# Kernel tuning notes

Hardware: AMD Instinct MI355X
Metric: run time of the kernel (lower is better)

The kernel has to match this reference:

```python
import jax, jax.numpy as jnp
import numpy as np

N = 10000
E = 160000
D = 512
EPS = 1e-5


def _lin_params(key, out_d, in_d, bias=True):
    k1, k2 = jax.random.split(key)
    s = 1.0 / np.sqrt(in_d)
    W = jax.random.uniform(k1, (out_d, in_d), jnp.float32, -s, s)
    if bias:
        b = jax.random.uniform(k2, (out_d,), jnp.float32, -s, s)
        return W, b
    return (W,)


def setup_inputs() -> dict:
    key = jax.random.key(0)
    ks = jax.random.split(key, 16)
    inp = {
        "x": jax.random.normal(ks[0], (N, D), jnp.float32),
        "edge_index": jax.random.randint(ks[1], (2, E), 0, N, jnp.int64),
    }
    ki = 2
    for l in range(3):
        Wp, bp = _lin_params(ks[ki], D, D); ki += 1
        Wl, bl = _lin_params(ks[ki], D, D); ki += 1
        (Wr,) = _lin_params(ks[ki], D, D, bias=False); ki += 1
        inp[f"Wp{l}"] = Wp; inp[f"bp{l}"] = bp
        inp[f"Wl{l}"] = Wl; inp[f"bl{l}"] = bl
        inp[f"Wr{l}"] = Wr
        if l < 2:  # ReLU+LayerNorm between convs
            inp[f"g{l}"] = jnp.ones((D,), jnp.float32)
            inp[f"be{l}"] = jnp.zeros((D,), jnp.float32)
    return inp


def _sage_conv(x, src, dst, Wp, bp, Wl, bl, Wr):
    # PyG SAGEConv with project=True: project+ReLU messages, mean-aggregate, lin_l + lin_r(root)
    h = jax.nn.relu(x @ Wp.T + bp)                      # [N, D] projected messages
    agg = jax.ops.segment_sum(h[src], dst, num_segments=N)   # gather + scatter-add
    cnt = jax.ops.segment_sum(jnp.ones((src.shape[0],), x.dtype), dst, num_segments=N)
    agg = agg / jnp.maximum(cnt, 1.0)[:, None]          # mean over incoming edges
    return agg @ Wl.T + bl + x @ Wr.T


def _relu_ln(x, g, b):
    x = jax.nn.relu(x)
    mu = jnp.mean(x, axis=-1, keepdims=True)
    var = jnp.mean(jnp.square(x - mu), axis=-1, keepdims=True)
    return (x - mu) * jax.lax.rsqrt(var + EPS) * g + b


def reference(x, edge_index,
              Wp0, bp0, Wl0, bl0, Wr0, g0, be0,
              Wp1, bp1, Wl1, bl1, Wr1, g1, be1,
              Wp2, bp2, Wl2, bl2, Wr2):
    src, dst = edge_index[0], edge_index[1]
    x = _sage_conv(x, src, dst, Wp0, bp0, Wl0, bl0, Wr0)
    x = _relu_ln(x, g0, be0)
    x = _sage_conv(x, src, dst, Wp1, bp1, Wl1, bl1, Wr1)
    x = _relu_ln(x, g1, be1)
    x = _sage_conv(x, src, dst, Wp2, bp2, Wl2, bl2, Wr2)
    return x
```

## Files before the change

kernel.cpp:

```cpp
#include <hip/hip_runtime.h>
#include <cstdint>

#define D 512
#define TM 128
#define TN 128
#define BK 32
#define CAP 64

typedef unsigned short u16;
typedef __bf16 bf16x8 __attribute__((ext_vector_type(8)));
typedef float f32x4 __attribute__((ext_vector_type(4)));

__device__ __forceinline__ float bf2f(u16 u) {
    unsigned int x = ((unsigned int)u) << 16;
    return __builtin_bit_cast(float, x);
}
__device__ __forceinline__ u16 f2bf(float f) {
    unsigned int x = __builtin_bit_cast(unsigned int, f);
    x += 0x7fffu + ((x >> 16) & 1u);
    return (u16)(x >> 16);
}

__device__ __forceinline__ void gload16(const u16* g, u16* l) {
    __builtin_amdgcn_global_load_lds(
        (const __attribute__((address_space(1))) void*)(uintptr_t)g,
        (__attribute__((address_space(3))) void*)(unsigned int)(uintptr_t)l,
        16, 0, 0);
}

__device__ __forceinline__ bool is_bf16(const u16* xraw) {
    int lane = threadIdx.x & 63;
    u16 u = xraw[2 * lane];
    int e = (u >> 7) & 0xFF;
    unsigned long long b = __ballot(e >= 110 && e <= 129);
    return __popcll(b) >= 32;
}
__device__ __forceinline__ bool is_i64(const int* eraw) {
    int lane = threadIdx.x & 63;
    unsigned long long b = __ballot(eraw[2 * lane + 1] == 0);
    return __popcll(b) >= 32;
}

__global__ __launch_bounds__(256) void convert_x(
    const void* __restrict__ src, u16* __restrict__ out)
{
    bool bf = is_bf16((const u16*)src);
    int i = (blockIdx.x * 256 + threadIdx.x) * 8;
    if (bf) {
        *(uint4*)(out + i) = *(const uint4*)((const u16*)src + i);
    } else {
        const float* f = (const float*)src + i;
        float4 a = *(const float4*)f;
        float4 b = *(const float4*)(f + 4);
        u16 r[8] = {f2bf(a.x), f2bf(a.y), f2bf(a.z), f2bf(a.w),
                    f2bf(b.x), f2bf(b.y), f2bf(b.z), f2bf(b.w)};
        *(uint4*)(out + i) = *(uint4*)r;
    }
}

struct Ptrs9  { const void* p[9];  };
struct Ptrs10 { const void* p[10]; };

__global__ __launch_bounds__(256) void convert_wb(
    Ptrs9 s, Ptrs10 v, u16* __restrict__ wout, float* __restrict__ vout,
    const u16* __restrict__ xraw)
{
    bool bf = is_bf16(xraw);
    int m = blockIdx.y;
    if (m < 9) {
        const void* src = s.p[m];
        u16* o = wout + (size_t)m * D * D;
        int i = (blockIdx.x * 256 + threadIdx.x) * 8;
        if (bf) {
            *(uint4*)(o + i) = *(const uint4*)((const u16*)src + i);
        } else {
            const float* f = (const float*)src + i;
            float4 a = *(const float4*)f;
            float4 b = *(const float4*)(f + 4);
            u16 r[8] = {f2bf(a.x), f2bf(a.y), f2bf(a.z), f2bf(a.w),
                        f2bf(b.x), f2bf(b.y), f2bf(b.z), f2bf(b.w)};
            *(uint4*)(o + i) = *(uint4*)r;
        }
    } else if (blockIdx.x == 0) {
        for (int b = 0; b < 10; b++) {
            const void* src = v.p[b];
            for (int j = threadIdx.x * 2; j < threadIdx.x * 2 + 2; j++) {
                float val = bf ? bf2f(((const u16*)src)[j]) : ((const float*)src)[j];
                vout[b * 512 + j] = val;
            }
        }
    }
}

__global__ void build_bucket(const int* __restrict__ eraw,
                             int* __restrict__ cnt, u16* __restrict__ bucket,
                             int E, int Nn)
{
    bool i64 = is_i64(eraw);
    int e = blockIdx.x * 256 + threadIdx.x;
    if (e < E) {
        int s, d;
        if (i64) { s = eraw[2 * e]; d = eraw[2 * (E + e)]; }
        else     { s = eraw[e];     d = eraw[E + e]; }
        s = min(max(s, 0), Nn - 1);
        d = min(max(d, 0), Nn - 1);
        int p = atomicAdd(&cnt[d], 1);
        if (p < CAP) bucket[(size_t)d * CAP + p] = (u16)s;
    }
}

template <int NPASS, bool RELU, bool FINAL>
__global__ __launch_bounds__(256) void gemm_bt(
    const u16* __restrict__ A0, const u16* __restrict__ B0,
    const u16* __restrict__ A1, const u16* __restrict__ B1,
    const float* __restrict__ bias, void* __restrict__ Cout,
    const u16* __restrict__ xraw, int M)
{
    __shared__ __align__(16) u16 sA[TM * BK];
    __shared__ __align__(16) u16 sB[TN * BK];

    const int t    = threadIdx.x;
    const int m0   = blockIdx.x * TM;
    const int n0   = blockIdx.y * TN;
    const int wave = t >> 6, lane = t & 63;
    const int wm   = wave >> 1, wn = wave & 1;
    const int lrow = lane & 15, quad = lane >> 4;

    const bool out_bf16 = FINAL ? is_bf16(xraw) : true;

    f32x4 acc[4][4];
#pragma unroll
    for (int i = 0; i < 4; i++)
#pragma unroll
        for (int j = 0; j < 4; j++)
#pragma unroll
            for (int r = 0; r < 4; r++) acc[i][j][r] = 0.f;

    const int cA  = (t & 3) * 8;
    const int rA0 = min(m0 + (t >> 2),      M - 1);
    const int rA1 = min(m0 + 64 + (t >> 2), M - 1);
    const int rB0 = n0 + (t >> 2);
    const int rB1 = n0 + 64 + (t >> 2);

#pragma unroll 1
    for (int p = 0; p < NPASS; p++) {
        const u16* A = p ? A1 : A0;
        const u16* B = p ? B1 : B0;
        const u16* gA0 = A + (size_t)rA0 * D + cA;
        const u16* gA1 = A + (size_t)rA1 * D + cA;
        const u16* gB0 = B + (size_t)rB0 * D + cA;
        const u16* gB1 = B + (size_t)rB1 * D + cA;

#pragma unroll 1
        for (int k0 = 0; k0 < D; k0 += BK) {
            gload16(gA0 + k0, &sA[(size_t)t * 8]);
            gload16(gA1 + k0, &sA[(size_t)(t + 256) * 8]);
            gload16(gB0 + k0, &sB[(size_t)t * 8]);
            gload16(gB1 + k0, &sB[(size_t)(t + 256) * 8]);
            __syncthreads();

            bf16x8 af[4], bfr[4];
#pragma unroll
            for (int mi = 0; mi < 4; mi++)
                af[mi] = *(const bf16x8*)&sA[(wm * 64 + mi * 16 + lrow) * BK + quad * 8];
#pragma unroll
            for (int ni = 0; ni < 4; ni++)
                bfr[ni] = *(const bf16x8*)&sB[(wn * 64 + ni * 16 + lrow) * BK + quad * 8];
#pragma unroll
            for (int mi = 0; mi < 4; mi++)
#pragma unroll
                for (int ni = 0; ni < 4; ni++)
                    acc[mi][ni] = __builtin_amdgcn_mfma_f32_16x16x32_bf16(
                        af[mi], bfr[ni], acc[mi][ni], 0, 0, 0);
            __syncthreads();
        }
    }

#pragma unroll
    for (int ni = 0; ni < 4; ni++) {
        int col = n0 + wn * 64 + ni * 16 + lrow;
        float bv = bias[col];
#pragma unroll
        for (int mi = 0; mi < 4; mi++) {
            int row0 = m0 + wm * 64 + mi * 16 + quad * 4;
#pragma unroll
            for (int r = 0; r < 4; r++) {
                int row = row0 + r;
                if (row < M) {
                    float v = acc[mi][ni][r] + bv;
                    if (RELU) v = fmaxf(v, 0.f);
                    if (!FINAL || out_bf16)
                        ((u16*)Cout)[(size_t)row * D + col] = f2bf(v);
                    else
                        ((float*)Cout)[(size_t)row * D + col] = v;
                }
            }
        }
    }
}

__global__ __launch_bounds__(256) void aggregate(
    const u16* __restrict__ h, const int* __restrict__ cnt,
    const u16* __restrict__ bucket, u16* __restrict__ agg, int M)
{
    const int w = threadIdx.x >> 6, lane = threadIdx.x & 63;
    const int n = blockIdx.x * 4 + w;

    __shared__ u16 sidx[4][CAP];
    int deg = 0, dd = 0;
    if (n < M) {
        deg = cnt[n];
        dd  = min(deg, CAP);
        if (lane < dd) sidx[w][lane] = bucket[(size_t)n * CAP + lane];
    }
    __syncthreads();
    if (n >= M) return;

    float a[8] = {0.f, 0.f, 0.f, 0.f, 0.f, 0.f, 0.f, 0.f};
    int i = 0;
    for (; i + 4 <= dd; i += 4) {
        uint4 v0 = *(const uint4*)(h + (size_t)sidx[w][i]     * D + lane * 8);
        uint4 v1 = *(const uint4*)(h + (size_t)sidx[w][i + 1] * D + lane * 8);
        uint4 v2 = *(const uint4*)(h + (size_t)sidx[w][i + 2] * D + lane * 8);
        uint4 v3 = *(const uint4*)(h + (size_t)sidx[w][i + 3] * D + lane * 8);
        const unsigned int* u0 = (const unsigned int*)&v0;
        const unsigned int* u1 = (const unsigned int*)&v1;
        const unsigned int* u2 = (const unsigned int*)&v2;
        const unsigned int* u3 = (const unsigned int*)&v3;
#pragma unroll
        for (int j = 0; j < 4; j++) {
            a[2 * j]     += bf2f((u16)(u0[j] & 0xffffu)) + bf2f((u16)(u1[j] & 0xffffu))
                          + bf2f((u16)(u2[j] & 0xffffu)) + bf2f((u16)(u3[j] & 0xffffu));
            a[2 * j + 1] += bf2f((u16)(u0[j] >> 16)) + bf2f((u16)(u1[j] >> 16))
                          + bf2f((u16)(u2[j] >> 16)) + bf2f((u16)(u3[j] >> 16));
        }
    }
    for (; i < dd; i++) {
        uint4 v0 = *(const uint4*)(h + (size_t)sidx[w][i] * D + lane * 8);
        const unsigned int* u0 = (const unsigned int*)&v0;
#pragma unroll
        for (int j = 0; j < 4; j++) {
            a[2 * j]     += bf2f((u16)(u0[j] & 0xffffu));
            a[2 * j + 1] += bf2f((u16)(u0[j] >> 16));
        }
    }

    float inv = 1.f / fmaxf((float)deg, 1.f);
    u16 r[8];
#pragma unroll
    for (int j = 0; j < 8; j++) r[j] = f2bf(a[j] * inv);
    *(uint4*)(agg + (size_t)n * D + lane * 8) = *(uint4*)r;
}

__global__ __launch_bounds__(256) void relu_ln(
    const u16* __restrict__ y, const float* __restrict__ g, const float* __restrict__ be,
    u16* __restrict__ out, int M)
{
    const int row  = blockIdx.x * 4 + (threadIdx.x >> 6);
    const int lane = threadIdx.x & 63;
    if (row >= M) return;

    typedef short s16x8 __attribute__((ext_vector_type(8)));
    s16x8 v = *(const s16x8*)(y + (size_t)row * D + lane * 8);
    float f[8], s = 0.f, s2 = 0.f;
#pragma unroll
    for (int i = 0; i < 8; i++) {
        float x = bf2f((u16)v[i]);
        x = fmaxf(x, 0.f);
        f[i] = x; s += x; s2 += x * x;
    }
#pragma unroll
    for (int off = 32; off >= 1; off >>= 1) {
        s  += __shfl_xor(s, off);
        s2 += __shfl_xor(s2, off);
    }
    float mean = s * (1.f / 512.f);
    float var  = s2 * (1.f / 512.f) - mean * mean;
    float rstd = rsqrtf(var + 1e-5f);

    s16x8 res;
#pragma unroll
    for (int i = 0; i < 8; i++) {
        float o = (f[i] - mean) * rstd * g[lane * 8 + i] + be[lane * 8 + i];
        res[i] = (short)f2bf(o);
    }
    *(s16x8*)(out + (size_t)row * D + lane * 8) = res;
}

extern "C" void kernel_launch(void* const* d_in, const int* in_sizes, int n_in,
                              void* d_out, int out_size, void* d_ws, size_t ws_size,
                              hipStream_t stream)
{
    const int M = in_sizes[0] / D;
    const int E = in_sizes[1] / 2;
    const void* xraw = d_in[0];
    const int*  eraw = (const int*)d_in[1];

    const void *Wp[3], *bp[3], *Wl[3], *bl[3], *Wr[3], *g[2], *be[2];
    int idx = 2;
    for (int l = 0; l < 3; l++) {
        Wp[l] = d_in[idx++]; bp[l] = d_in[idx++];
        Wl[l] = d_in[idx++]; bl[l] = d_in[idx++];
        Wr[l] = d_in[idx++];
        if (l < 2) { g[l] = d_in[idx++]; be[l] = d_in[idx++]; }
    }

    char* w = (char*)d_ws;
    auto alloc = [&](size_t bytes) { void* p = w; w += (bytes + 255) & ~(size_t)255; return p; };
    u16*   xb     = (u16*)  alloc((size_t)M * D * 2);
    u16*   h      = (u16*)  alloc((size_t)M * D * 2);
    u16*   agg    = (u16*)  alloc((size_t)M * D * 2);
    u16*   Wb     = (u16*)  alloc((size_t)9 * D * D * 2);
    float* vecf   = (float*)alloc((size_t)10 * 512 * 4);
    int*   cnt    = (int*)  alloc((size_t)M * 4);
    u16*   bucket = (u16*)  alloc((size_t)M * CAP * 2);

    convert_x<<<dim3(M * D / (256 * 8)), dim3(256), 0, stream>>>(xraw, xb);

    Ptrs9 mats;
    const void* morder[9] = {Wp[0], Wl[0], Wr[0], Wp[1], Wl[1], Wr[1], Wp[2], Wl[2], Wr[2]};
    for (int i = 0; i < 9; i++) mats.p[i] = morder[i];
    Ptrs10 vecs;
    const void* vorder[10] = {bp[0], bl[0], g[0], be[0], bp[1], bl[1], g[1], be[1], bp[2], bl[2]};
    for (int i = 0; i < 10; i++) vecs.p[i] = vorder[i];
    convert_wb<<<dim3(D * D / (256 * 8), 10), dim3(256), 0, stream>>>(
        mats, vecs, Wb, vecf, (const u16*)xraw);

    hipMemsetAsync(cnt, 0, (size_t)M * 4, stream);
    build_bucket<<<dim3((E + 255) / 256), dim3(256), 0, stream>>>(eraw, cnt, bucket, E, M);

    const u16* WM[9]; for (int i = 0; i < 9; i++) WM[i] = Wb + (size_t)i * D * D;
    const float* VB[10]; for (int i = 0; i < 10; i++) VB[i] = vecf + (size_t)i * 512;

    u16* yb = (u16*)d_out;
    dim3 gg((M + TM - 1) / TM, D / TN);
    const u16* xin = xb;
    for (int l = 0; l < 3; l++) {
        gemm_bt<1, true, false><<<gg, dim3(256), 0, stream>>>(
            xin, WM[l * 3 + 0], xin, WM[l * 3 + 0], VB[l * 4 + 0], h, (const u16*)xraw, M);
        aggregate<<<dim3((M + 3) / 4), dim3(256), 0, stream>>>(h, cnt, bucket, agg, M);
        if (l < 2) {
            gemm_bt<2, false, false><<<gg, dim3(256), 0, stream>>>(
                agg, WM[l * 3 + 1], xin, WM[l * 3 + 2], VB[l * 4 + 1], yb, (const u16*)xraw, M);
            relu_ln<<<dim3((M + 3) / 4), dim3(256), 0, stream>>>(
                yb, VB[l * 4 + 2], VB[l * 4 + 3], xb, M);
            xin = xb;
        } else {
            gemm_bt<2, false, true><<<gg, dim3(256), 0, stream>>>(
                agg, WM[l * 3 + 1], xin, WM[l * 3 + 2], VB[l * 4 + 1], d_out, (const u16*)xraw, M);
        }
    }
}
```

Measured before the change: 381.0 us.

## Fold LayerNorm into next-layer weights and fuse prep kernels

Removes the separate relu_ln kernel. The gamma scale is folded into the next layer's Wp and Wr weights, and beta is folded into bias vectors computed in a prep pass. The ReLU'd output of the second GEMM is stored together with per-row sum and sum-of-squares gathered through atomics, and the next GEMMs apply mean and rstd in their epilogue. It also merges the x conversion, weight conversion and edge bucketing into one grid-stride prep kernel, and halves TN to 64 for more blocks. The costs are row-stat atomics, a serial 512-length dot per thread in prep, and a change in numerics, since LN is now applied after a bf16 GEMM on un-normalized inputs.

```diff
diff --git a/kernel.cpp b/kernel.cpp
--- a/kernel.cpp
+++ b/kernel.cpp
@@ -3,7 +3,7 @@
 
 #define D 512
 #define TM 128
-#define TN 128
+#define TN 64
 #define BK 32
 #define CAP 64
 
@@ -20,14 +20,15 @@
     x += 0x7fffu + ((x >> 16) & 1u);
     return (u16)(x >> 16);
 }
-
+__device__ __forceinline__ float loadf(const void* p, int i, bool bf) {
+    return bf ? bf2f(((const u16*)p)[i]) : ((const float*)p)[i];
+}
 __device__ __forceinline__ void gload16(const u16* g, u16* l) {
     __builtin_amdgcn_global_load_lds(
         (const __attribute__((address_space(1))) void*)(uintptr_t)g,
         (__attribute__((address_space(3))) void*)(unsigned int)(uintptr_t)l,
         16, 0, 0);
 }
-
 __device__ __forceinline__ bool is_bf16(const u16* xraw) {
     int lane = threadIdx.x & 63;
     u16 u = xraw[2 * lane];
@@ -41,80 +42,108 @@
     return __popcll(b) >= 32;
 }
 
-__global__ __launch_bounds__(256) void convert_x(
-    const void* __restrict__ src, u16* __restrict__ out)
+struct PrepArgs {
+    const u16* xraw; const int* eraw;
+    const void* W[9];
+    const void* V[10];
+    u16* xb; u16* Wb; float* vecf;
+    int* cnt; u16* bucket;
+    int M, E;
+};
+
+__global__ __launch_bounds__(256) void prep(PrepArgs a)
 {
-    bool bf = is_bf16((const u16*)src);
-    int i = (blockIdx.x * 256 + threadIdx.x) * 8;
-    if (bf) {
-        *(uint4*)(out + i) = *(const uint4*)((const u16*)src + i);
-    } else {
-        const float* f = (const float*)src + i;
-        float4 a = *(const float4*)f;
-        float4 b = *(const float4*)(f + 4);
-        u16 r[8] = {f2bf(a.x), f2bf(a.y), f2bf(a.z), f2bf(a.w),
-                    f2bf(b.x), f2bf(b.y), f2bf(b.z), f2bf(b.w)};
-        *(uint4*)(out + i) = *(uint4*)r;
-    }
-}
-
-struct Ptrs9  { const void* p[9];  };
-struct Ptrs10 { const void* p[10]; };
-
-__global__ __launch_bounds__(256) void convert_wb(
-    Ptrs9 s, Ptrs10 v, u16* __restrict__ wout, float* __restrict__ vout,
-    const u16* __restrict__ xraw)
-{
-    bool bf = is_bf16(xraw);
-    int m = blockIdx.y;
-    if (m < 9) {
-        const void* src = s.p[m];
-        u16* o = wout + (size_t)m * D * D;
-        int i = (blockIdx.x * 256 + threadIdx.x) * 8;
+    const bool bf  = is_bf16(a.xraw);
+    const bool i64 = is_i64(a.eraw);
+    const int gt = blockIdx.x * 256 + threadIdx.x;
+    const int gs = gridDim.x * 256;
+
+    const int nx = a.M * D / 8;
+    for (int i = gt; i < nx; i += gs) {
         if (bf) {
-            *(uint4*)(o + i) = *(const uint4*)((const u16*)src + i);
+            *(uint4*)(a.xb + i * 8) = *(const uint4*)(a.xraw + i * 8);
         } else {
-            const float* f = (const float*)src + i;
-            float4 a = *(const float4*)f;
-            float4 b = *(const float4*)(f + 4);
-            u16 r[8] = {f2bf(a.x), f2bf(a.y), f2bf(a.z), f2bf(a.w),
-                        f2bf(b.x), f2bf(b.y), f2bf(b.z), f2bf(b.w)};
-            *(uint4*)(o + i) = *(uint4*)r;
-        }
-    } else if (blockIdx.x == 0) {
-        for (int b = 0; b < 10; b++) {
-            const void* src = v.p[b];
-            for (int j = threadIdx.x * 2; j < threadIdx.x * 2 + 2; j++) {
-                float val = bf ? bf2f(((const u16*)src)[j]) : ((const float*)src)[j];
-                vout[b * 512 + j] = val;
-            }
-        }
-    }
-}
-
-__global__ void build_bucket(const int* __restrict__ eraw,
-                             int* __restrict__ cnt, u16* __restrict__ bucket,
-                             int E, int Nn)
-{
-    bool i64 = is_i64(eraw);
-    int e = blockIdx.x * 256 + threadIdx.x;
-    if (e < E) {
+            const float* f = (const float*)a.xraw + i * 8;
+            float4 p = *(const float4*)f, q = *(const float4*)(f + 4);
+            u16 r[8] = {f2bf(p.x), f2bf(p.y), f2bf(p.z), f2bf(p.w),
+                        f2bf(q.x), f2bf(q.y), f2bf(q.z), f2bf(q.w)};
+            *(uint4*)(a.xb + i * 8) = *(uint4*)r;
+        }
+    }
+
+    for (int i = gt; i < 9 * 32768; i += gs) {
+        int m = i >> 15, j = i & 32767;
+        const void* gsrc = nullptr;
+        if (m == 3 || m == 5) gsrc = a.V[2];
+        else if (m == 6 || m == 8) gsrc = a.V[6];
+        const void* src = a.W[m];
+        int c0 = (j * 8) & 511;
+        float v[8];
+        if (bf) {
+            const u16* s = (const u16*)src + j * 8;
+#pragma unroll
+            for (int e = 0; e < 8; e++) v[e] = bf2f(s[e]);
+        } else {
+            const float* s = (const float*)src + j * 8;
+#pragma unroll
+            for (int e = 0; e < 8; e++) v[e] = s[e];
+        }
+        if (gsrc) {
+#pragma unroll
+            for (int e = 0; e < 8; e++) v[e] *= loadf(gsrc, c0 + e, bf);
+        }
+        u16 r[8];
+#pragma unroll
+        for (int e = 0; e < 8; e++) r[e] = f2bf(v[e]);
+        *(uint4*)(a.Wb + (size_t)m * D * D + j * 8) = *(uint4*)r;
+    }
+
+    for (int e = gt; e < 10 * 512; e += gs) {
+        int t = e >> 9, n = e & 511;
+        float outv;
+        if (t == 0)      outv = loadf(a.V[0], n, bf);
+        else if (t == 1) outv = loadf(a.V[1], n, bf);
+        else {
+            int q = t - 2;
+            const int wi[8] = {3, 3, 5, 5, 6, 6, 8, 8};
+            const void* wraw = a.W[wi[q]];
+            const void* dotv = (q < 4) ? ((q & 1) ? a.V[3] : a.V[2])
+                                       : ((q & 1) ? a.V[7] : a.V[6]);
+            float acc = 0.f;
+            if (bf) {
+                const u16* wr = (const u16*)wraw + (size_t)n * 512;
+                for (int k = 0; k < 512; k++) acc += bf2f(wr[k]) * loadf(dotv, k, bf);
+            } else {
+                const float* wr = (const float*)wraw + (size_t)n * 512;
+                for (int k = 0; k < 512; k++) acc += wr[k] * loadf(dotv, k, bf);
+            }
+            if (q & 1) {
+                const void* braw = (q == 1) ? a.V[4] : (q == 3) ? a.V[5]
+                                 : (q == 5) ? a.V[8] : a.V[9];
+                acc += loadf(braw, n, bf);
+            }
+            outv = acc;
+        }
+        a.vecf[t * 512 + n] = outv;
+    }
+
+    for (int e2 = gt; e2 < a.E; e2 += gs) {
         int s, d;
-        if (i64) { s = eraw[2 * e]; d = eraw[2 * (E + e)]; }
-        else     { s = eraw[e];     d = eraw[E + e]; }
-        s = min(max(s, 0), Nn - 1);
-        d = min(max(d, 0), Nn - 1);
-        int p = atomicAdd(&cnt[d], 1);
-        if (p < CAP) bucket[(size_t)d * CAP + p] = (u16)s;
-    }
-}
-
-template <int NPASS, bool RELU, bool FINAL>
-__global__ __launch_bounds__(256) void gemm_bt(
-    const u16* __restrict__ A0, const u16* __restrict__ B0,
-    const u16* __restrict__ A1, const u16* __restrict__ B1,
-    const float* __restrict__ bias, void* __restrict__ Cout,
-    const u16* __restrict__ xraw, int M)
+        if (i64) { s = a.eraw[2 * e2]; d = a.eraw[2 * (a.E + e2)]; }
+        else     { s = a.eraw[e2];     d = a.eraw[a.E + e2]; }
+        s = min(max(s, 0), a.M - 1);
+        d = min(max(d, 0), a.M - 1);
+        int p = atomicAdd(&a.cnt[d], 1);
+        if (p < CAP) a.bucket[(size_t)d * CAP + p] = (u16)s;
+    }
+}
+
+template <bool LNIN>
+__global__ __launch_bounds__(256) void gemm1k(
+    const u16* __restrict__ A, const u16* __restrict__ W,
+    const float* __restrict__ bias, const float* __restrict__ svec,
+    const float* __restrict__ mu, const float* __restrict__ m2,
+    u16* __restrict__ hout, int M)
 {
     __shared__ __align__(16) u16 sA[TM * BK];
     __shared__ __align__(16) u16 sB[TN * BK];
@@ -126,73 +155,212 @@
     const int wm   = wave >> 1, wn = wave & 1;
     const int lrow = lane & 15, quad = lane >> 4;
 
+    float rstd[4][4], nmu[4][4];
+    if (LNIN) {
+#pragma unroll
+        for (int mi = 0; mi < 4; mi++)
+#pragma unroll
+            for (int r = 0; r < 4; r++) {
+                int row = min(m0 + wm * 64 + mi * 16 + quad * 4 + r, M - 1);
+                float mean = mu[row] * (1.f / 512.f);
+                float var  = m2[row] * (1.f / 512.f) - mean * mean;
+                float rs   = rsqrtf(fmaxf(var, 0.f) + 1e-5f);
+                rstd[mi][r] = rs;
+                nmu[mi][r]  = -mean * rs;
+            }
+    }
+
+    f32x4 acc[4][2];
+#pragma unroll
+    for (int i = 0; i < 4; i++)
+#pragma unroll
+        for (int j = 0; j < 2; j++)
+#pragma unroll
+            for (int r = 0; r < 4; r++) acc[i][j][r] = 0.f;
+
+    const int cA    = (t & 3) * 8;
+    const int rowA0 = min(m0 + (t >> 2),      M - 1);
+    const int rowA1 = min(m0 + 64 + (t >> 2), M - 1);
+    const int rowB  = n0 + (t >> 2);
+    const u16* gA0 = A + (size_t)rowA0 * D + cA;
+    const u16* gA1 = A + (size_t)rowA1 * D + cA;
+    const u16* gB  = W + (size_t)rowB  * D + cA;
+
+#pragma unroll 1
+    for (int k0 = 0; k0 < D; k0 += BK) {
+        gload16(gA0 + k0, &sA[(size_t)t * 8]);
+        gload16(gA1 + k0, &sA[(size_t)(t + 256) * 8]);
+        gload16(gB  + k0, &sB[(size_t)t * 8]);
+        __syncthreads();
+        bf16x8 af[4], bfr[2];
+#pragma unroll
+        for (int mi = 0; mi < 4; mi++)
+            af[mi] = *(const bf16x8*)&sA[(wm * 64 + mi * 16 + lrow) * BK + quad * 8];
+#pragma unroll
+        for (int ni = 0; ni < 2; ni++)
+            bfr[ni] = *(const bf16x8*)&sB[(wn * 32 + ni * 16 + lrow) * BK + quad * 8];
+#pragma unroll
+        for (int mi = 0; mi < 4; mi++)
+#pragma unroll
+            for (int ni = 0; ni < 2; ni++)
+                acc[mi][ni] = __builtin_amdgcn_mfma_f32_16x16x32_bf16(
+                    af[mi], bfr[ni], acc[mi][ni], 0, 0, 0);
+        __syncthreads();
+    }
+
+#pragma unroll
+    for (int ni = 0; ni < 2; ni++) {
+        int col = n0 + wn * 32 + ni * 16 + lrow;
+        float bv = bias[col];
+        float sv = LNIN ? svec[col] : 0.f;
+#pragma unroll
+        for (int mi = 0; mi < 4; mi++) {
+            int row0 = m0 + wm * 64 + mi * 16 + quad * 4;
+#pragma unroll
+            for (int r = 0; r < 4; r++) {
+                int row = row0 + r;
+                if (row < M) {
+                    float v = LNIN ? rstd[mi][r] * acc[mi][ni][r] + nmu[mi][r] * sv + bv
+                                   : acc[mi][ni][r] + bv;
+                    hout[(size_t)row * D + col] = f2bf(fmaxf(v, 0.f));
+                }
+            }
+        }
+    }
+}
+
+template <bool LNIN, bool STATS, bool FINAL>
+__global__ __launch_bounds__(256) void gemm2k(
+    const u16* __restrict__ A0, const u16* __restrict__ W0,
+    const u16* __restrict__ A1, const u16* __restrict__ W1,
+    const float* __restrict__ bias, const float* __restrict__ s2vec,
+    const float* __restrict__ mu_in, const float* __restrict__ m2_in,
+    float* __restrict__ mu_out, float* __restrict__ m2_out,
+    void* __restrict__ out, const u16* __restrict__ xraw, int M)
+{
+    __shared__ __align__(16) u16 sA[TM * BK];
+    __shared__ __align__(16) u16 sB[TN * BK];
+
+    const int t    = threadIdx.x;
+    const int m0   = blockIdx.x * TM;
+    const int n0   = blockIdx.y * TN;
+    const int wave = t >> 6, lane = t & 63;
+    const int wm   = wave >> 1, wn = wave & 1;
+    const int lrow = lane & 15, quad = lane >> 4;
+
     const bool out_bf16 = FINAL ? is_bf16(xraw) : true;
 
-    f32x4 acc[4][4];
+    float rstd[4][4], nmu[4][4], inv[4][4];
+    if (LNIN) {
+#pragma unroll
+        for (int mi = 0; mi < 4; mi++)
+#pragma unroll
+            for (int r = 0; r < 4; r++) {
+                int row = min(m0 + wm * 64 + mi * 16 + quad * 4 + r, M - 1);
+                float mean = mu_in[row] * (1.f / 512.f);
+                float var  = m2_in[row] * (1.f / 512.f) - mean * mean;
+                float s    = sqrtf(fmaxf(var, 0.f) + 1e-5f);
+                float rs   = 1.f / s;
+                rstd[mi][r] = rs;
+                inv[mi][r]  = s;
+                nmu[mi][r]  = -mean * rs;
+            }
+    }
+
+    f32x4 acc[4][2];
 #pragma unroll
     for (int i = 0; i < 4; i++)
 #pragma unroll
-        for (int j = 0; j < 4; j++)
+        for (int j = 0; j < 2; j++)
 #pragma unroll
             for (int r = 0; r < 4; r++) acc[i][j][r] = 0.f;
 
-    const int cA  = (t & 3) * 8;
-    const int rA0 = min(m0 + (t >> 2),      M - 1);
-    const int rA1 = min(m0 + 64 + (t >> 2), M - 1);
-    const int rB0 = n0 + (t >> 2);
-    const int rB1 = n0 + 64 + (t >> 2);
+    const int cA    = (t & 3) * 8;
+    const int rowA0 = min(m0 + (t >> 2),      M - 1);
+    const int rowA1 = min(m0 + 64 + (t >> 2), M - 1);
+    const int rowB  = n0 + (t >> 2);
 
 #pragma unroll 1
-    for (int p = 0; p < NPASS; p++) {
+    for (int p = 0; p < 2; p++) {
         const u16* A = p ? A1 : A0;
-        const u16* B = p ? B1 : B0;
-        const u16* gA0 = A + (size_t)rA0 * D + cA;
-        const u16* gA1 = A + (size_t)rA1 * D + cA;
-        const u16* gB0 = B + (size_t)rB0 * D + cA;
-        const u16* gB1 = B + (size_t)rB1 * D + cA;
+        const u16* W = p ? W1 : W0;
+        if (LNIN && p == 1) {
+#pragma unroll
+            for (int mi = 0; mi < 4; mi++)
+#pragma unroll
+                for (int ni = 0; ni < 2; ni++)
+#pragma unroll
+                    for (int r = 0; r < 4; r++) acc[mi][ni][r] *= inv[mi][r];
+        }
+        const u16* gA0 = A + (size_t)rowA0 * D + cA;
+        const u16* gA1 = A + (size_t)rowA1 * D + cA;
+        const u16* gB  = W + (size_t)rowB  * D + cA;
 
 #pragma unroll 1
         for (int k0 = 0; k0 < D; k0 += BK) {
             gload16(gA0 + k0, &sA[(size_t)t * 8]);
             gload16(gA1 + k0, &sA[(size_t)(t + 256) * 8]);
-            gload16(gB0 + k0, &sB[(size_t)t * 8]);
-            gload16(gB1 + k0, &sB[(size_t)(t + 256) * 8]);
+            gload16(gB  + k0, &sB[(size_t)t * 8]);
             __syncthreads();
-
-            bf16x8 af[4], bfr[4];
+            bf16x8 af[4], bfr[2];
 #pragma unroll
             for (int mi = 0; mi < 4; mi++)
                 af[mi] = *(const bf16x8*)&sA[(wm * 64 + mi * 16 + lrow) * BK + quad * 8];
 #pragma unroll
-            for (int ni = 0; ni < 4; ni++)
-                bfr[ni] = *(const bf16x8*)&sB[(wn * 64 + ni * 16 + lrow) * BK + quad * 8];
+            for (int ni = 0; ni < 2; ni++)
+                bfr[ni] = *(const bf16x8*)&sB[(wn * 32 + ni * 16 + lrow) * BK + quad * 8];
 #pragma unroll
             for (int mi = 0; mi < 4; mi++)
 #pragma unroll
-                for (int ni = 0; ni < 4; ni++)
+                for (int ni = 0; ni < 2; ni++)
                     acc[mi][ni] = __builtin_amdgcn_mfma_f32_16x16x32_bf16(
                         af[mi], bfr[ni], acc[mi][ni], 0, 0, 0);
             __syncthreads();
         }
     }
 
-#pragma unroll
-    for (int ni = 0; ni < 4; ni++) {
-        int col = n0 + wn * 64 + ni * 16 + lrow;
-        float bv = bias[col];
-#pragma unroll
-        for (int mi = 0; mi < 4; mi++) {
-            int row0 = m0 + wm * 64 + mi * 16 + quad * 4;
-#pragma unroll
-            for (int r = 0; r < 4; r++) {
-                int row = row0 + r;
-                if (row < M) {
-                    float v = acc[mi][ni][r] + bv;
-                    if (RELU) v = fmaxf(v, 0.f);
-                    if (!FINAL || out_bf16)
-                        ((u16*)Cout)[(size_t)row * D + col] = f2bf(v);
-                    else
-                        ((float*)Cout)[(size_t)row * D + col] = v;
+    float bvv[2], svv[2];
+#pragma unroll
+    for (int ni = 0; ni < 2; ni++) {
+        int col = n0 + wn * 32 + ni * 16 + lrow;
+        bvv[ni] = bias[col];
+        svv[ni] = LNIN ? s2vec[col] : 0.f;
+    }
+
+#pragma unroll
+    for (int mi = 0; mi < 4; mi++) {
+#pragma unroll
+        for (int r = 0; r < 4; r++) {
+            int row = m0 + wm * 64 + mi * 16 + quad * 4 + r;
+            float sr = 0.f, s2r = 0.f;
+#pragma unroll
+            for (int ni = 0; ni < 2; ni++) {
+                int col = n0 + wn * 32 + ni * 16 + lrow;
+                float v = acc[mi][ni][r];
+                if (LNIN) v = rstd[mi][r] * v + nmu[mi][r] * svv[ni] + bvv[ni];
+                else      v += bvv[ni];
+                if (FINAL) {
+                    if (row < M) {
+                        if (out_bf16) ((u16*)out)[(size_t)row * D + col] = f2bf(v);
+                        else          ((float*)out)[(size_t)row * D + col] = v;
+                    }
+                } else {
+                    u16 zb = f2bf(fmaxf(v, 0.f));
+                    float z = bf2f(zb);
+                    if (row < M) ((u16*)out)[(size_t)row * D + col] = zb;
+                    sr  += z;
+                    s2r += z * z;
+                }
+            }
+            if (STATS) {
+#pragma unroll
+                for (int off = 1; off <= 8; off <<= 1) {
+                    sr  += __shfl_xor(sr, off);
+                    s2r += __shfl_xor(s2r, off);
+                }
+                if (lrow == 0 && row < M) {
+                    atomicAdd(&mu_out[row], sr);
+                    atomicAdd(&m2_out[row], s2r);
                 }
             }
         }
@@ -245,46 +413,11 @@
         }
     }
 
-    float inv = 1.f / fmaxf((float)deg, 1.f);
+    float invd = 1.f / fmaxf((float)deg, 1.f);
     u16 r[8];
 #pragma unroll
-    for (int j = 0; j < 8; j++) r[j] = f2bf(a[j] * inv);
+    for (int j = 0; j < 8; j++) r[j] = f2bf(a[j] * invd);
     *(uint4*)(agg + (size_t)n * D + lane * 8) = *(uint4*)r;
-}
-
-__global__ __launch_bounds__(256) void relu_ln(
-    const u16* __restrict__ y, const float* __restrict__ g, const float* __restrict__ be,
-    u16* __restrict__ out, int M)
-{
-    const int row  = blockIdx.x * 4 + (threadIdx.x >> 6);
-    const int lane = threadIdx.x & 63;
-    if (row >= M) return;
-
-    typedef short s16x8 __attribute__((ext_vector_type(8)));
-    s16x8 v = *(const s16x8*)(y + (size_t)row * D + lane * 8);
-    float f[8], s = 0.f, s2 = 0.f;
-#pragma unroll
-    for (int i = 0; i < 8; i++) {
-        float x = bf2f((u16)v[i]);
-        x = fmaxf(x, 0.f);
-        f[i] = x; s += x; s2 += x * x;
-    }
-#pragma unroll
-    for (int off = 32; off >= 1; off >>= 1) {
-        s  += __shfl_xor(s, off);
-        s2 += __shfl_xor(s2, off);
-    }
-    float mean = s * (1.f / 512.f);
-    float var  = s2 * (1.f / 512.f) - mean * mean;
-    float rstd = rsqrtf(var + 1e-5f);
-
-    s16x8 res;
-#pragma unroll
-    for (int i = 0; i < 8; i++) {
-        float o = (f[i] - mean) * rstd * g[lane * 8 + i] + be[lane * 8 + i];
-        res[i] = (short)f2bf(o);
-    }
-    *(s16x8*)(out + (size_t)row * D + lane * 8) = res;
 }
 
 extern "C" void kernel_launch(void* const* d_in, const int* in_sizes, int n_in,
@@ -293,61 +426,69 @@
 {
     const int M = in_sizes[0] / D;
     const int E = in_sizes[1] / 2;
-    const void* xraw = d_in[0];
-    const int*  eraw = (const int*)d_in[1];
-
-    const void *Wp[3], *bp[3], *Wl[3], *bl[3], *Wr[3], *g[2], *be[2];
-    int idx = 2;
-    for (int l = 0; l < 3; l++) {
-        Wp[l] = d_in[idx++]; bp[l] = d_in[idx++];
-        Wl[l] = d_in[idx++]; bl[l] = d_in[idx++];
-        Wr[l] = d_in[idx++];
-        if (l < 2) { g[l] = d_in[idx++]; be[l] = d_in[idx++]; }
+
+    PrepArgs a;
+    a.xraw = (const u16*)d_in[0];
+    a.eraw = (const int*)d_in[1];
+    {
+        int idx = 2;
+        for (int l = 0; l < 3; l++) {
+            a.W[l * 3 + 0] = d_in[idx++];
+            a.V[l * 4 + 0] = d_in[idx++];
+            a.W[l * 3 + 1] = d_in[idx++];
+            a.V[l * 4 + 1] = d_in[idx++];
+            a.W[l * 3 + 2] = d_in[idx++];
+            if (l < 2) {
+                a.V[l * 4 + 2] = d_in[idx++];
+                a.V[l * 4 + 3] = d_in[idx++];
+            }
+        }
     }
 
     char* w = (char*)d_ws;
     auto alloc = [&](size_t bytes) { void* p = w; w += (bytes + 255) & ~(size_t)255; return p; };
-    u16*   xb     = (u16*)  alloc((size_t)M * D * 2);
-    u16*   h      = (u16*)  alloc((size_t)M * D * 2);
-    u16*   agg    = (u16*)  alloc((size_t)M * D * 2);
-    u16*   Wb     = (u16*)  alloc((size_t)9 * D * D * 2);
-    float* vecf   = (float*)alloc((size_t)10 * 512 * 4);
-    int*   cnt    = (int*)  alloc((size_t)M * 4);
-    u16*   bucket = (u16*)  alloc((size_t)M * CAP * 2);
-
-    convert_x<<<dim3(M * D / (256 * 8)), dim3(256), 0, stream>>>(xraw, xb);
-
-    Ptrs9 mats;
-    const void* morder[9] = {Wp[0], Wl[0], Wr[0], Wp[1], Wl[1], Wr[1], Wp[2], Wl[2], Wr[2]};
-    for (int i = 0; i < 9; i++) mats.p[i] = morder[i];
-    Ptrs10 vecs;
-    const void* vorder[10] = {bp[0], bl[0], g[0], be[0], bp[1], bl[1], g[1], be[1], bp[2], bl[2]};
-    for (int i = 0; i < 10; i++) vecs.p[i] = vorder[i];
-    convert_wb<<<dim3(D * D / (256 * 8), 10), dim3(256), 0, stream>>>(
-        mats, vecs, Wb, vecf, (const u16*)xraw);
-
-    hipMemsetAsync(cnt, 0, (size_t)M * 4, stream);
-    build_bucket<<<dim3((E + 255) / 256), dim3(256), 0, stream>>>(eraw, cnt, bucket, E, M);
-
-    const u16* WM[9]; for (int i = 0; i < 9; i++) WM[i] = Wb + (size_t)i * D * D;
-    const float* VB[10]; for (int i = 0; i < 10; i++) VB[i] = vecf + (size_t)i * 512;
-
-    u16* yb = (u16*)d_out;
+    u16*   xb   = (u16*)  alloc((size_t)M * D * 2);
+    u16*   h    = (u16*)  alloc((size_t)M * D * 2);
+    u16*   aggb = (u16*)  alloc((size_t)M * D * 2);
+    u16*   z0   = (u16*)  alloc((size_t)M * D * 2);
+    u16*   z1   = (u16*)  alloc((size_t)M * D * 2);
+    u16*   Wb   = (u16*)  alloc((size_t)9 * D * D * 2);
+    float* vecf = (float*)alloc((size_t)10 * 512 * 4);
+    int*   cnt  = (int*)  alloc((size_t)M * 4);
+    float* mu0  = (float*)alloc((size_t)M * 4);
+    float* m20  = (float*)alloc((size_t)M * 4);
+    float* mu1  = (float*)alloc((size_t)M * 4);
+    float* m21  = (float*)alloc((size_t)M * 4);
+    u16* bucket = (u16*)  alloc((size_t)M * CAP * 2);
+
+    a.xb = xb; a.Wb = Wb; a.vecf = vecf; a.cnt = cnt; a.bucket = bucket;
+    a.M = M; a.E = E;
+
+    hipMemsetAsync(cnt, 0, (size_t)((char*)bucket - (char*)cnt), stream);
+    prep<<<dim3(1024), dim3(256), 0, stream>>>(a);
+
+    const size_t DD = (size_t)D * D;
     dim3 gg((M + TM - 1) / TM, D / TN);
-    const u16* xin = xb;
-    for (int l = 0; l < 3; l++) {
-        gemm_bt<1, true, false><<<gg, dim3(256), 0, stream>>>(
-            xin, WM[l * 3 + 0], xin, WM[l * 3 + 0], VB[l * 4 + 0], h, (const u16*)xraw, M);
-        aggregate<<<dim3((M + 3) / 4), dim3(256), 0, stream>>>(h, cnt, bucket, agg, M);
-        if (l < 2) {
-            gemm_bt<2, false, false><<<gg, dim3(256), 0, stream>>>(
-                agg, WM[l * 3 + 1], xin, WM[l * 3 + 2], VB[l * 4 + 1], yb, (const u16*)xraw, M);
-            relu_ln<<<dim3((M + 3) / 4), dim3(256), 0, stream>>>(
-                yb, VB[l * 4 + 2], VB[l * 4 + 3], xb, M);
-            xin = xb;
-        } else {
-            gemm_bt<2, false, true><<<gg, dim3(256), 0, stream>>>(
-                agg, WM[l * 3 + 1], xin, WM[l * 3 + 2], VB[l * 4 + 1], d_out, (const u16*)xraw, M);
-        }
-    }
-}
+    dim3 ga((M + 3) / 4);
+
+    gemm1k<false><<<gg, dim3(256), 0, stream>>>(
+        xb, Wb + 0 * DD, vecf + 0 * 512, nullptr, nullptr, nullptr, h, M);
+    aggregate<<<ga, dim3(256), 0, stream>>>(h, cnt, bucket, aggb, M);
+    gemm2k<false, true, false><<<gg, dim3(256), 0, stream>>>(
+        aggb, Wb + 1 * DD, xb, Wb + 2 * DD, vecf + 1 * 512, nullptr,
+        nullptr, nullptr, mu0, m20, z0, a.xraw, M);
+
+    gemm1k<true><<<gg, dim3(256), 0, stream>>>(
+        z0, Wb + 3 * DD, vecf + 3 * 512, vecf + 2 * 512, mu0, m20, h, M);
+    aggregate<<<ga, dim3(256), 0, stream>>>(h, cnt, bucket, aggb, M);
+    gemm2k<true, true, false><<<gg, dim3(256), 0, stream>>>(
+        aggb, Wb + 4 * DD, z0, Wb + 5 * DD, vecf + 5 * 512, vecf + 4 * 512,
+        mu0, m20, mu1, m21, z1, a.xraw, M);
+
+    gemm1k<true><<<gg, dim3(256), 0, stream>>>(
+        z1, Wb + 6 * DD, vecf + 7 * 512, vecf + 6 * 512, mu1, m21, h, M);
+    aggregate<<<ga, dim3(256), 0, stream>>>(h, cnt, bucket, aggb, M);
+    gemm2k<true, false, true><<<gg, dim3(256), 0, stream>>>(
+        aggb, Wb + 7 * DD, z1, Wb + 8 * DD, vecf + 9 * 512, vecf + 8 * 512,
+        mu1, m21, nullptr, nullptr, d_out, a.xraw, M);
+}
```

After: 368.3 us. -3.3%, faster.
